# Kernel tuning notes

Hardware: AMD Instinct MI355X
Metric: run time of the kernel (lower is better)

The kernel has to match this reference:

```python
import jax, jax.numpy as jnp
import numpy as np

B = 2048
G = 8
C = B * G  # 16384


def setup_inputs() -> dict:
    key = jax.random.key(0)
    k1, k2 = jax.random.split(key)
    student_scores = jax.random.normal(k1, (B, C), dtype=jnp.float32)
    teacher_targets = jax.random.uniform(k2, (B, G), dtype=jnp.float32)
    return {
        "student_scores": student_scores,
        "teacher_targets": teacher_targets,
        "group_size": G,
    }


def reference(student_scores, teacher_targets, group_size):
    b = student_scores.shape[0]
    rows = jnp.arange(b)
    labels = rows * group_size  # base target column per row
    neg = jnp.finfo(student_scores.dtype).min
    mask = jnp.zeros_like(student_scores)
    loss = jnp.zeros((), dtype=student_scores.dtype)
    # group_size is small and fixed (e.g. 8): Python loop over it is fine.
    for i in range(group_size):
        tgt = labels + i                       # [B]
        s = student_scores + mask              # [B, C], previously-used targets masked to -inf
        lse = jax.nn.logsumexp(s, axis=-1)     # [B]
        picked = s[rows, tgt]                  # [B] logits at the current target
        ce = lse - picked                      # per-row cross entropy, reduction='none'
        loss = loss + jnp.mean(teacher_targets[:, i] * ce)
        mask = mask.at[rows, tgt].set(neg)
    return loss
```

## Files before the change

### kernel.cpp

```cpp
#include <hip/hip_runtime.h>


#define BB 2048
#define CC 16384
#define GG 8
#define NT 256
#define PER_THREAD (CC / NT)
#define NBATCH 2
#define NVEC 8

typedef float f32x4 __attribute__((ext_vector_type(4)));

__global__ __launch_bounds__(NT, 8) void kd_row_kernel(
    const float* __restrict__ scores,
    const float* __restrict__ teacher,
    float* __restrict__ partial)
{
    const int row = blockIdx.x;
    const int tid = threadIdx.x;
    const float* rp = scores + (size_t)row * CC;
    const f32x4* rp4 = reinterpret_cast<const f32x4*>(rp);

    float t = 0.0f, w = 0.0f;
    if (tid < GG) {
        t = rp[row * GG + tid];
        w = teacher[row * GG + tid];
    }

    float s0 = 0.0f, s1 = 0.0f;
    f32x4 v[NVEC];
#pragma unroll
    for (int b = 0; b < NBATCH; ++b) {
#pragma unroll
        for (int i = 0; i < NVEC; ++i) v[i] = rp4[(b * NVEC + i) * NT + tid];
        __builtin_amdgcn_sched_barrier(0);
#pragma unroll
        for (int i = 0; i < NVEC; ++i) {
            s0 += __expf(v[i].x) + __expf(v[i].y);
            s1 += __expf(v[i].z) + __expf(v[i].w);
        }
    }
    float s = s0 + s1;

#pragma unroll
    for (int off = 32; off >= 1; off >>= 1) s += __shfl_xor(s, off);

    __shared__ float ss[NT / 64];
    const int wave = tid >> 6;
    const int lane = tid & 63;
    if (lane == 0) ss[wave] = s;
    __syncthreads();

    if (tid < GG) {
        float S = 0.0f;
#pragma unroll
        for (int q = 0; q < NT / 64; ++q) S += ss[q];

        float e = __expf(t);
        float p = e;
#pragma unroll
        for (int off = 1; off < GG; off <<= 1) {
            float o = __shfl_up(p, off, GG);
            if (tid >= off) p += o;
        }
        float S2 = S - (p - e);
        float contrib = w * (__logf(S2) - t);
#pragma unroll
        for (int off = GG / 2; off >= 1; off >>= 1)
            contrib += __shfl_xor(contrib, off, GG);
        if (tid == 0) partial[row] = contrib;
    }
}

__global__ __launch_bounds__(256) void kd_reduce_kernel(
    const float* __restrict__ partial,
    float* __restrict__ out)
{
    const int tid = threadIdx.x;
    const f32x4* p4 = reinterpret_cast<const f32x4*>(partial);
    f32x4 a = p4[tid];
    f32x4 b = p4[tid + 256];
    float s = (a.x + a.y + a.z + a.w) + (b.x + b.y + b.z + b.w);
#pragma unroll
    for (int off = 32; off >= 1; off >>= 1) s += __shfl_xor(s, off);
    __shared__ float ws[4];
    const int wave = tid >> 6;
    const int lane = tid & 63;
    if (lane == 0) ws[wave] = s;
    __syncthreads();
    if (tid == 0) out[0] = (ws[0] + ws[1] + ws[2] + ws[3]) * (1.0f / BB);
}

extern "C" void kernel_launch(void* const* d_in, const int* in_sizes, int n_in,
                              void* d_out, int out_size, void* d_ws, size_t ws_size,
                              hipStream_t stream) {
    const float* scores  = (const float*)d_in[0];
    const float* teacher = (const float*)d_in[1];
    float* partial = (float*)d_ws;
    float* out = (float*)d_out;

    kd_row_kernel<<<BB, NT, 0, stream>>>(scores, teacher, partial);
    kd_reduce_kernel<<<1, 256, 0, stream>>>(partial, out);
}
```

Baseline: 26.52 us.

## Fuse final reduction into row kernel via packed counter-plus-fixed-point atomics

Removes the separate single-block reduce kernel. Each row block instead adds its contribution as a fixed-point value packed with a count into one of 32 strided 64-bit atomic slots. The last block in each slot forwards that slot's sum to a global slot, and the last slot writes the final mean. This saves a kernel launch and its serial tail, but adds a memset launch and atomic traffic. It also assumes contributions are non-negative and fit the fixed-point range, since a negative value cast to unsigned would corrupt the sum.

```diff
diff --git a/kernel.cpp b/kernel.cpp
--- a/kernel.cpp
+++ b/kernel.cpp
@@ -5,16 +5,22 @@
 #define CC 16384
 #define GG 8
 #define NT 256
-#define PER_THREAD (CC / NT)
 #define NBATCH 2
 #define NVEC 8
 
+#define CNT_SHIFT 56
+#define VAL_MASK ((1ull << CNT_SHIFT) - 1)
+#define FIX_SCALE 268435456.0
+#define LINES 32
+#define LINE_STRIDE 8
+
 typedef float f32x4 __attribute__((ext_vector_type(4)));
 
-__global__ __launch_bounds__(NT, 8) void kd_row_kernel(
+__global__ __launch_bounds__(NT, 8) void kd_fused_kernel(
     const float* __restrict__ scores,
     const float* __restrict__ teacher,
-    float* __restrict__ partial)
+    unsigned long long* __restrict__ acc,
+    float* __restrict__ out)
 {
     const int row = blockIdx.x;
     const int tid = threadIdx.x;
@@ -68,27 +74,23 @@
 #pragma unroll
         for (int off = GG / 2; off >= 1; off >>= 1)
             contrib += __shfl_xor(contrib, off, GG);
-        if (tid == 0) partial[row] = contrib;
+
+        if (tid == 0) {
+            unsigned long long myv =
+                (unsigned long long)((double)contrib * FIX_SCALE);
+            unsigned long long pk = (1ull << CNT_SHIFT) | myv;
+            unsigned long long old = atomicAdd(&acc[(row >> 6) * LINE_STRIDE], pk);
+            if ((old >> CNT_SHIFT) == 63ull) {
+                unsigned long long line_total = (old & VAL_MASK) + myv;
+                unsigned long long gold = atomicAdd(&acc[LINES * LINE_STRIDE],
+                                                    (1ull << CNT_SHIFT) | line_total);
+                if ((gold >> CNT_SHIFT) == (unsigned long long)(LINES - 1)) {
+                    unsigned long long total = (gold & VAL_MASK) + line_total;
+                    out[0] = (float)((double)total * (1.0 / (FIX_SCALE * (double)BB)));
+                }
+            }
+        }
     }
-}
-
-__global__ __launch_bounds__(256) void kd_reduce_kernel(
-    const float* __restrict__ partial,
-    float* __restrict__ out)
-{
-    const int tid = threadIdx.x;
-    const f32x4* p4 = reinterpret_cast<const f32x4*>(partial);
-    f32x4 a = p4[tid];
-    f32x4 b = p4[tid + 256];
-    float s = (a.x + a.y + a.z + a.w) + (b.x + b.y + b.z + b.w);
-#pragma unroll
-    for (int off = 32; off >= 1; off >>= 1) s += __shfl_xor(s, off);
-    __shared__ float ws[4];
-    const int wave = tid >> 6;
-    const int lane = tid & 63;
-    if (lane == 0) ws[wave] = s;
-    __syncthreads();
-    if (tid == 0) out[0] = (ws[0] + ws[1] + ws[2] + ws[3]) * (1.0f / BB);
 }
 
 extern "C" void kernel_launch(void* const* d_in, const int* in_sizes, int n_in,
@@ -96,9 +98,10 @@
                               hipStream_t stream) {
     const float* scores  = (const float*)d_in[0];
     const float* teacher = (const float*)d_in[1];
-    float* partial = (float*)d_ws;
+    unsigned long long* acc = (unsigned long long*)d_ws;
     float* out = (float*)d_out;
 
-    kd_row_kernel<<<BB, NT, 0, stream>>>(scores, teacher, partial);
-    kd_reduce_kernel<<<1, 256, 0, stream>>>(partial, out);
+    hipMemsetAsync(d_ws, 0, (LINES * LINE_STRIDE + 1) * sizeof(unsigned long long),
+                   stream);
+    kd_fused_kernel<<<BB, NT, 0, stream>>>(scores, teacher, acc, out);
 }
```

Result: slower. 32.52 us (+22.6%).
